# Performance work log

Hardware: AMD Instinct MI355X
Metric: run time of the kernel (lower is better)

Reference implementation:

```python
import jax, jax.numpy as jnp
from jax import lax
import numpy as np

N = 4
ALPHA_AP = 0.85
ALPHA_DS = 0.1
ALPHA_LR = 1.0
C1 = 0.01 ** 2
C2 = 0.03 ** 2


def resize_ac(img, nh, nw):
    # bilinear resize, align_corners=True (matches F.interpolate(..., align_corners=True))
    B, C, H, W = img.shape
    ys = jnp.linspace(0.0, H - 1.0, nh)
    xs = jnp.linspace(0.0, W - 1.0, nw)
    y0 = jnp.floor(ys).astype(jnp.int32)
    y1 = jnp.minimum(y0 + 1, H - 1)
    x0 = jnp.floor(xs).astype(jnp.int32)
    x1 = jnp.minimum(x0 + 1, W - 1)
    wy = (ys - y0).astype(img.dtype)[None, None, :, None]
    wx = (xs - x0).astype(img.dtype)[None, None, None, :]
    top = img[:, :, y0, :] * (1.0 - wy) + img[:, :, y1, :] * wy
    return top[:, :, :, x0] * (1.0 - wx) + top[:, :, :, x1] * wx


def build_pyramid(img):
    B, C, H, W = img.shape
    pyr = [img]
    for i in range(N - 1):
        r = 2 ** (i + 1)
        pyr.append(resize_ac(pyr[i], H // r, W // r))  # resize previous level, as in torch code
    return pyr


def x_grad(img):
    # replicate-pad right then diff -> last column is exactly zero
    g = img[:, :, :, :-1] - img[:, :, :, 1:]
    return jnp.concatenate([g, jnp.zeros_like(img[:, :, :, :1])], axis=3)


def y_grad(img):
    g = img[:, :, :-1, :] - img[:, :, 1:, :]
    return jnp.concatenate([g, jnp.zeros_like(img[:, :, :1, :])], axis=2)


def avgpool3(x):
    # AvgPool2d(3, 1), VALID padding
    return lax.reduce_window(x, 0.0, lax.add, (1, 1, 3, 3), (1, 1, 1, 1), 'VALID') / 9.0


def grid_sample_zeros(img, gx, gy):
    # bilinear grid_sample, padding_mode='zeros', align_corners=True
    B, C, H, W = img.shape
    x = (gx + 1.0) * 0.5 * (W - 1)
    y = (gy + 1.0) * 0.5 * (H - 1)
    x0 = jnp.floor(x)
    y0 = jnp.floor(y)

    def corner(xi, yi, w):
        valid = (xi >= 0) & (xi <= W - 1) & (yi >= 0) & (yi <= H - 1)
        xc = jnp.clip(xi, 0, W - 1).astype(jnp.int32)
        yc = jnp.clip(yi, 0, H - 1).astype(jnp.int32)
        vals = jax.vmap(lambda im, yy, xx: im[:, yy, xx])(img, yc, xc)  # [B,C,H,W]
        return vals * (w * valid.astype(img.dtype))[:, None]

    return (corner(x0, y0, (x0 + 1 - x) * (y0 + 1 - y))
            + corner(x0 + 1, y0, (x - x0) * (y0 + 1 - y))
            + corner(x0, y0 + 1, (x0 + 1 - x) * (y - y0))
            + corner(x0 + 1, y0 + 1, (x - x0) * (y - y0)))


def apply_disparity(img, disp):
    # standard Monodepth bilinear sampler: shift x_base in [0,1] by disp, grid_sample
    B, C, H, W = img.shape
    x_base = jnp.linspace(0.0, 1.0, W)[None, None, :]
    y_base = jnp.linspace(0.0, 1.0, H)[None, :, None]
    gx = 2.0 * (x_base + disp[:, 0]) - 1.0  # [B,H,W]
    gy = jnp.broadcast_to(2.0 * y_base - 1.0, gx.shape)
    return grid_sample_zeros(img, gx, gy)


def dssim(x, y):
    mu_x = avgpool3(x)
    mu_y = avgpool3(y)
    sig_x = avgpool3(x * x) - mu_x ** 2
    sig_y = avgpool3(y * y) - mu_y ** 2
    cov = avgpool3(x * y) - mu_x * mu_y
    ssim = ((2.0 * mu_x * mu_y + C1) * (2.0 * cov + C2)) / ((mu_x ** 2 + mu_y ** 2 + C1) * (sig_x + sig_y + C2))
    return jnp.mean(jnp.clip((1.0 - ssim) / 2.0, 0.0, 1.0))


def smoothness(disp, img, level):
    wx = jnp.exp(-jnp.mean(jnp.abs(x_grad(img)), axis=1, keepdims=True))
    wy = jnp.exp(-jnp.mean(jnp.abs(y_grad(img)), axis=1, keepdims=True))
    sx = x_grad(disp) * wx
    sy = y_grad(disp) * wy
    return jnp.mean(jnp.abs(sx) + jnp.abs(sy)) / (2 ** level)


def loss_forward(disps, left, right):
    lp = build_pyramid(left)
    rp = build_pyramid(right)
    dl = [d[:, 0:1] for d in disps]
    dr = [d[:, 1:2] for d in disps]
    left_est = [apply_disparity(rp[i], -dl[i]) for i in range(N)]
    right_est = [apply_disparity(lp[i], dr[i]) for i in range(N)]
    r2l_disp = [apply_disparity(dr[i], -dl[i]) for i in range(N)]
    l2r_disp = [apply_disparity(dl[i], dr[i]) for i in range(N)]
    # appearance matching (note: outer *ALPHA_AP matches the original's AP_loss*self.alpha_AP)
    AP = sum(ALPHA_AP * dssim(lp[i], left_est[i]) + (1.0 - ALPHA_AP) * jnp.mean(jnp.abs(lp[i] - left_est[i])) for i in range(N))
    AP = AP + sum(ALPHA_AP * dssim(rp[i], right_est[i]) + (1.0 - ALPHA_AP) * jnp.mean(jnp.abs(rp[i] - right_est[i])) for i in range(N))
    AP = AP * ALPHA_AP
    LR = sum(jnp.mean(jnp.abs(dl[i] - r2l_disp[i])) for i in range(N))
    LR = (LR + sum(jnp.mean(jnp.abs(dr[i] - l2r_disp[i])) for i in range(N))) * ALPHA_LR
    DS = sum(smoothness(dl[i], lp[i], i) for i in range(N))
    DS = (DS + sum(smoothness(dr[i], rp[i], i) for i in range(N))) * ALPHA_DS
    total = AP + LR + DS
    return total, AP, LR, DS


def setup_inputs() -> dict:
    key = jax.random.key(0)
    ks = jax.random.split(key, 6)
    B, H, W = 32, 256, 512
    inp = {}
    for i in range(N):
        h, w = H >> i, W >> i
        # normalized disparities in [0, 0.05) as in trained Monodepth
        inp[f'disp{i}'] = jax.random.uniform(ks[i], (B, 2, h, w), jnp.float32) * 0.05
    inp['left'] = jax.random.uniform(ks[4], (B, 3, H, W), jnp.float32)
    inp['right'] = jax.random.uniform(ks[5], (B, 3, H, W), jnp.float32)
    return inp


def reference(disp0, disp1, disp2, disp3, left, right):
    return loss_forward([disp0, disp1, disp2, disp3], left, right)
```

## Files before the change

### kernel.cpp

```cpp
#include <hip/hip_runtime.h>

#define BDIM 256
#define SH 16

struct LevelDesc {
    const float* lp; const float* rp; const float* dp;
    int H, W, nCW, nRS, nPerSide, waveBase;
};
struct AllParams { LevelDesc lv[4]; int totalWaves; };

__global__ void zero_acc_kernel(double* acc) {
    if (threadIdx.x < 32) acc[threadIdx.x] = 0.0;
}

__global__ void resize2_kernel(const float* __restrict__ sL, const float* __restrict__ sR,
                               float* __restrict__ dL, float* __restrict__ dR,
                               int BC, int Hs, int Ws, int Hd, int Wd) {
    long long half = (long long)BC * Hd * Wd;
    long long idx = (long long)blockIdx.x * blockDim.x + threadIdx.x;
    if (idx >= 2 * half) return;
    const float* src = (idx < half) ? sL : sR;
    float* dst = (idx < half) ? dL : dR;
    long long id = (idx < half) ? idx : idx - half;
    int i = (int)(id % Wd);
    long long t = id / Wd;
    int j = (int)(t % Hd);
    int bc = (int)(t / Hd);
    float stepy = (float)(Hs - 1) / (float)(Hd - 1);
    float stepx = (float)(Ws - 1) / (float)(Wd - 1);
    float y = j * stepy;
    float x = i * stepx;
    int y0 = (int)floorf(y);
    int y1 = min(y0 + 1, Hs - 1);
    int x0 = (int)floorf(x);
    int x1 = min(x0 + 1, Ws - 1);
    float wy = y - (float)y0;
    float wx = x - (float)x0;
    const float* s = src + (long long)bc * Hs * Ws;
    float t0 = s[(long long)y0 * Ws + x0] * (1.0f - wy) + s[(long long)y1 * Ws + x0] * wy;
    float t1 = s[(long long)y0 * Ws + x1] * (1.0f - wy) + s[(long long)y1 * Ws + x1] * wy;
    dst[id] = t0 * (1.0f - wx) + t1 * wx;
}

__device__ __forceinline__ float ssim_term(float Sx, float Sy, float Sxx, float Syy, float Sxy) {
    const float C1v = 0.0001f;
    const float C2v = 0.0009f;
    float mux = Sx * (1.0f / 9.0f), muy = Sy * (1.0f / 9.0f);
    float sigx = Sxx * (1.0f / 9.0f) - mux * mux;
    float sigy = Syy * (1.0f / 9.0f) - muy * muy;
    float cov  = Sxy * (1.0f / 9.0f) - mux * muy;
    float num = (2.0f * mux * muy + C1v) * (2.0f * cov + C2v);
    float den = (mux * mux + muy * muy + C1v) * (sigx + sigy + C2v);
    float v = (1.0f - num * __builtin_amdgcn_rcpf(den)) * 0.5f;
    return fminf(fmaxf(v, 0.0f), 1.0f);
}

struct RowVals {
    float d0, d1;
    float xv[3][2];
    float w00, w01, w10, w11;
    float dA, dB, dC, dD;
    float sA[3], sB[3], sC[3], sD[3];
};

__global__ void __launch_bounds__(BDIM)
mega_kernel(AllParams P, double* __restrict__ acc) {
    const int lane = threadIdx.x & 63;
    const int wid  = threadIdx.x >> 6;
    const int wId  = blockIdx.x * (BDIM / 64) + wid;
    const int w = min(wId, P.totalWaves - 1);

    int level = 0;
    if (w >= P.lv[1].waveBase) level = 1;
    if (w >= P.lv[2].waveBase) level = 2;
    if (w >= P.lv[3].waveBase) level = 3;
    LevelDesc L;
    if (level == 0) L = P.lv[0];
    else if (level == 1) L = P.lv[1];
    else if (level == 2) L = P.lv[2];
    else L = P.lv[3];

    int rel = w - L.waveBase;
    const int side = (rel >= L.nPerSide) ? 1 : 0;
    rel -= side * L.nPerSide;
    const int cw = rel % L.nCW; rel /= L.nCW;
    const int rs = rel % L.nRS;
    const int b  = rel / L.nRS;

    const int H = L.H, W = L.W;
    const long long HW = (long long)H * W;
    const unsigned HWu = (unsigned)HW;
    const float Wm1f = (float)(W - 1);
    const float sgn = side ? 1.0f : -1.0f;

    const float* xim = (side ? L.rp : L.lp) + (long long)b * 3 * HW;
    const float* sim = (side ? L.lp : L.rp) + (long long)b * 3 * HW;
    const float* dme = L.dp + (long long)b * 2 * HW + (side ? HW : 0);
    const float* dot = L.dp + (long long)b * 2 * HW + (side ? 0 : HW);

    const int base = cw * 126;
    const int c0 = base + 2 * lane;
    const int c1 = c0 + 1;
    const bool in0 = c0 < W, in1 = c1 < W;
    const int cc = min(c0, W - 2) >> 1;
    const float fc0 = (float)c0, fc1 = (float)c1;

    const bool lastW = (cw == L.nCW - 1);
    const bool own0 = in0 && (c0 < base + 126 || lastW);
    const bool own1 = in1 && (c1 < base + 126 || lastW);
    const bool ownS0 = own0 && (c0 <= W - 3);
    const bool ownS1 = own1 && (c1 <= W - 3);

    const int r0 = rs * SH;
    const int r1 = min(r0 + SH, H);
    const int jend = min(r1 + 1, H - 1);

    float Pst[3][5][2], Lst[3][5][2];
#pragma unroll
    for (int c = 0; c < 3; ++c)
#pragma unroll
        for (int s = 0; s < 5; ++s) { Pst[c][s][0] = 0.f; Pst[c][s][1] = 0.f;
                                      Lst[c][s][0] = 0.f; Lst[c][s][1] = 0.f; }
    float pd0 = 0.f, pd1 = 0.f;
    float pxv[3][2] = {{0.f,0.f},{0.f,0.f},{0.f,0.f}};

    float f_ss = 0.f, f_l1 = 0.f, f_lr = 0.f, f_ds = 0.f;

    auto load_dp = [&](int jj, float& o0, float& o1) {
        float2 dpair = ((const float2*)(dme + (unsigned)jj * (unsigned)W))[cc];
        o0 = dpair.x; o1 = dpair.y;
    };

    auto issue_gathers = [&](float di0, float di1, int jj, RowVals& R) {
        const unsigned ro = (unsigned)jj * (unsigned)W;
        R.d0 = di0; R.d1 = di1;
        float xq0 = fmaf(sgn * di0, Wm1f, fc0);
        float xq1 = fmaf(sgn * di1, Wm1f, fc1);
        float xf0 = floorf(xq0), xf1 = floorf(xq1);
        int g0 = (int)xf0, g1 = (int)xf1;
        float t0 = xq0 - xf0, t1 = xq1 - xf1;
        R.w00 = (g0 >= 0 && g0 < W)         ? 1.0f - t0 : 0.0f;
        R.w01 = (g0 >= -1 && g0 < W - 1)    ? t0        : 0.0f;
        R.w10 = (g1 >= 0 && g1 < W)         ? 1.0f - t1 : 0.0f;
        R.w11 = (g1 >= -1 && g1 < W - 1)    ? t1        : 0.0f;
        unsigned a0 = ro + (unsigned)min(max(g0, 0), W - 1);
        unsigned a1 = ro + (unsigned)min(max(g0 + 1, 0), W - 1);
        unsigned b0 = ro + (unsigned)min(max(g1, 0), W - 1);
        unsigned b1 = ro + (unsigned)min(max(g1 + 1, 0), W - 1);
        R.dA = dot[a0]; R.dB = dot[a1]; R.dC = dot[b0]; R.dD = dot[b1];
#pragma unroll
        for (int c = 0; c < 3; ++c) {
            const unsigned co = (unsigned)c * HWu;
            float2 xp2 = ((const float2*)(xim + co + ro))[cc];
            R.xv[c][0] = in0 ? xp2.x : 0.f;
            R.xv[c][1] = in1 ? xp2.y : 0.f;
            R.sA[c] = sim[co + a0]; R.sB[c] = sim[co + a1];
            R.sC[c] = sim[co + b0]; R.sD[c] = sim[co + b1];
        }
    };

    auto consume = [&](const RowVals& R, int j) {
        const float d0 = R.d0, d1 = R.d1;
        float wv0 = R.dA * R.w00 + R.dB * R.w01;
        float wv1 = R.dC * R.w10 + R.dD * R.w11;
        float xv[3][2], yv[3][2];
#pragma unroll
        for (int c = 0; c < 3; ++c) {
            xv[c][0] = R.xv[c][0]; xv[c][1] = R.xv[c][1];
            float ya = R.sA[c] * R.w00 + R.sB[c] * R.w01;
            float yb = R.sC[c] * R.w10 + R.sD[c] * R.w11;
            yv[c][0] = in0 ? ya : 0.f;
            yv[c][1] = in1 ? yb : 0.f;
        }

        const bool rowOwn = j < r1;
        if (rowOwn) {
            if (own0) {
                f_l1 += fabsf(xv[0][0] - yv[0][0]) + fabsf(xv[1][0] - yv[1][0]) + fabsf(xv[2][0] - yv[2][0]);
                f_lr += fabsf(d0 - wv0);
            }
            if (own1) {
                f_l1 += fabsf(xv[0][1] - yv[0][1]) + fabsf(xv[1][1] - yv[1][1]) + fabsf(xv[2][1] - yv[2][1]);
                f_lr += fabsf(d1 - wv1);
            }
        }

        {
            float dn  = __shfl_down(d0, 1);
            float xn0 = __shfl_down(xv[0][0], 1);
            float xn1 = __shfl_down(xv[1][0], 1);
            float xn2 = __shfl_down(xv[2][0], 1);
            if (rowOwn) {
                if (own0 && c0 < W - 1) {
                    float g = fabsf(xv[0][0] - xv[0][1]) + fabsf(xv[1][0] - xv[1][1]) + fabsf(xv[2][0] - xv[2][1]);
                    f_ds += fabsf((d0 - d1) * __expf(-g * (1.0f / 3.0f)));
                }
                if (own1 && c1 < W - 1) {
                    float g = fabsf(xv[0][1] - xn0) + fabsf(xv[1][1] - xn1) + fabsf(xv[2][1] - xn2);
                    f_ds += fabsf((d1 - dn) * __expf(-g * (1.0f / 3.0f)));
                }
            }
        }
        if (j > r0 && (j - 1) < r1) {
            if (own0) {
                float g = fabsf(pxv[0][0] - xv[0][0]) + fabsf(pxv[1][0] - xv[1][0]) + fabsf(pxv[2][0] - xv[2][0]);
                f_ds += fabsf((pd0 - d0) * __expf(-g * (1.0f / 3.0f)));
            }
            if (own1) {
                float g = fabsf(pxv[0][1] - xv[0][1]) + fabsf(pxv[1][1] - xv[1][1]) + fabsf(pxv[2][1] - xv[2][1]);
                f_ds += fabsf((pd1 - d1) * __expf(-g * (1.0f / 3.0f)));
            }
        }
        pd0 = d0; pd1 = d1;
#pragma unroll
        for (int c = 0; c < 3; ++c) { pxv[c][0] = xv[c][0]; pxv[c][1] = xv[c][1]; }

        const bool emit = (j >= r0 + 2);
#pragma unroll
        for (int c = 0; c < 3; ++c) {
            float cs[5][2];
#pragma unroll
            for (int p = 0; p < 2; ++p) {
                float cx = xv[c][p], cy = yv[c][p];
                float v5[5] = {cx, cy, cx * cx, cy * cy, cx * cy};
#pragma unroll
                for (int s = 0; s < 5; ++s) {
                    cs[s][p] = Pst[c][s][p] + v5[s];
                    Pst[c][s][p] = Lst[c][s][p] + v5[s];
                    Lst[c][s][p] = v5[s];
                }
            }
            if (emit) {
                float w0s[5], w1s[5];
#pragma unroll
                for (int s = 0; s < 5; ++s) {
                    float n0 = __shfl_down(cs[s][0], 1);
                    float n1 = __shfl_down(cs[s][1], 1);
                    w0s[s] = cs[s][0] + cs[s][1] + n0;
                    w1s[s] = cs[s][1] + n0 + n1;
                }
                float ts0 = ssim_term(w0s[0], w0s[1], w0s[2], w0s[3], w0s[4]);
                float ts1 = ssim_term(w1s[0], w1s[1], w1s[2], w1s[3], w1s[4]);
                f_ss += (ownS0 ? ts0 : 0.f) + (ownS1 ? ts1 : 0.f);
            }
        }
    };

    RowVals A, B;
    float dq0, dq1, dn0, dn1;
    load_dp(r0, dq0, dq1);
    load_dp(min(r0 + 1, jend), dn0, dn1);
    issue_gathers(dq0, dq1, r0, A);

    int j = r0;
    for (;;) {
        float dp20, dp21;
        load_dp(min(j + 2, jend), dp20, dp21);
        if (j < jend) issue_gathers(dn0, dn1, j + 1, B);
        consume(A, j);
        dn0 = dp20; dn1 = dp21;
        if (++j > jend) break;

        load_dp(min(j + 2, jend), dp20, dp21);
        if (j < jend) issue_gathers(dn0, dn1, j + 1, A);
        consume(B, j);
        dn0 = dp20; dn1 = dp21;
        if (++j > jend) break;
    }

#pragma unroll
    for (int o = 32; o > 0; o >>= 1) {
        f_ss += __shfl_down(f_ss, o);
        f_l1 += __shfl_down(f_l1, o);
        f_lr += __shfl_down(f_lr, o);
        f_ds += __shfl_down(f_ds, o);
    }
    __shared__ float red[BDIM / 64][4];
    __shared__ int meta[2];
    if (threadIdx.x == 0) { meta[0] = level; meta[1] = side; }
    if (lane == 0) {
        red[wid][0] = f_ss; red[wid][1] = f_l1;
        red[wid][2] = f_lr; red[wid][3] = f_ds;
    }
    __syncthreads();
    if (threadIdx.x < 4) {
        int t = threadIdx.x;
        double s = (double)red[0][t] + (double)red[1][t]
                 + (double)red[2][t] + (double)red[3][t];
        atomicAdd(acc + t * 8 + meta[1] * 4 + meta[0], s);
    }
}

__global__ void finalize_kernel(const double* __restrict__ acc, float* __restrict__ out) {
    const int B = 32, H0 = 256, W0 = 512;
    double AP = 0.0, LR = 0.0, DS = 0.0;
    for (int i = 0; i < 4; ++i) {
        int h = H0 >> i, w = W0 >> i;
        double nss = (double)B * 3.0 * (double)(h - 2) * (double)(w - 2);
        double nl1 = (double)B * 3.0 * (double)h * (double)w;
        double nd  = (double)B * (double)h * (double)w;
        AP += 0.85 * (acc[0 + i] / nss) + 0.15 * (acc[8 + i] / nl1);
        AP += 0.85 * (acc[4 + i] / nss) + 0.15 * (acc[12 + i] / nl1);
        LR += acc[16 + i] / nd + acc[20 + i] / nd;
        double sc = 1.0 / (double)(1 << i);
        DS += (acc[24 + i] / nd) * sc + (acc[28 + i] / nd) * sc;
    }
    AP *= 0.85;
    DS *= 0.1;
    double total = AP + LR + DS;
    out[0] = (float)total;
    out[1] = (float)AP;
    out[2] = (float)LR;
    out[3] = (float)DS;
}

extern "C" void kernel_launch(void* const* d_in, const int* in_sizes, int n_in,
                              void* d_out, int out_size, void* d_ws, size_t ws_size,
                              hipStream_t stream) {
    const int B = 32, H0 = 256, W0 = 512;
    const float* dsp[4];
    for (int i = 0; i < 4; ++i) dsp[i] = (const float*)d_in[i];
    const float* left  = (const float*)d_in[4];
    const float* right = (const float*)d_in[5];
    float* out = (float*)d_out;

    double* acc = (double*)d_ws;
    float* buf = (float*)((char*)d_ws + 256);

    const float* lp[4];
    const float* rp[4];
    float* lpm[4];
    float* rpm[4];
    lp[0] = left; rp[0] = right;
    float* cur = buf;
    for (int i = 1; i < 4; ++i) { lpm[i] = cur; cur += (long long)B * 3 * (H0 >> i) * (W0 >> i); }
    for (int i = 1; i < 4; ++i) { rpm[i] = cur; cur += (long long)B * 3 * (H0 >> i) * (W0 >> i); }
    for (int i = 1; i < 4; ++i) { lp[i] = lpm[i]; rp[i] = rpm[i]; }

    zero_acc_kernel<<<1, 64, 0, stream>>>(acc);

    for (int i = 1; i < 4; ++i) {
        int Hs = H0 >> (i - 1), Ws = W0 >> (i - 1);
        int Hd = H0 >> i, Wd = W0 >> i;
        long long half = (long long)B * 3 * Hd * Wd;
        int g = (int)((2 * half + BDIM - 1) / BDIM);
        resize2_kernel<<<g, BDIM, 0, stream>>>(
            lp[i - 1], rp[i - 1], lpm[i], rpm[i], B * 3, Hs, Ws, Hd, Wd);
    }

    AllParams P;
    int wb = 0;
    for (int i = 0; i < 4; ++i) {
        int h = H0 >> i, w = W0 >> i;
        LevelDesc& L = P.lv[i];
        L.lp = lp[i]; L.rp = rp[i]; L.dp = dsp[i];
        L.H = h; L.W = w;
        L.nCW = (w - 2 + 125) / 126;
        L.nRS = h / SH;
        L.nPerSide = B * L.nRS * L.nCW;
        L.waveBase = wb;
        wb += 2 * L.nPerSide;
    }
    P.totalWaves = wb;
    int blocks = (wb + (BDIM / 64) - 1) / (BDIM / 64);
    mega_kernel<<<blocks, BDIM, 0, stream>>>(P, acc);

    finalize_kernel<<<1, 1, 0, stream>>>(acc, out);
}
```

Baseline: 308.6 us.

## Pack SSIM math into float2 vectors, use DPP shifts, uniform base pointers, fold zeroing

```diff
diff --git a/kernel.cpp b/kernel.cpp
--- a/kernel.cpp
+++ b/kernel.cpp
@@ -2,6 +2,8 @@
 
 #define BDIM 256
 #define SH 16
+
+typedef float v2f __attribute__((ext_vector_type(2)));
 
 struct LevelDesc {
     const float* lp; const float* rp; const float* dp;
@@ -9,13 +11,26 @@
 };
 struct AllParams { LevelDesc lv[4]; int totalWaves; };
 
-__global__ void zero_acc_kernel(double* acc) {
-    if (threadIdx.x < 32) acc[threadIdx.x] = 0.0;
-}
+__device__ __forceinline__ float dpp_shl1(float x) {
+    int r = __builtin_amdgcn_update_dpp(0, __float_as_int(x), 0x130, 0xF, 0xF, true);
+    return __int_as_float(r);
+}
+
+__device__ __forceinline__ const float* uptr(const float* p) {
+    unsigned long long u = (unsigned long long)p;
+    unsigned lo = __builtin_amdgcn_readfirstlane((unsigned)u);
+    unsigned hi = __builtin_amdgcn_readfirstlane((unsigned)(u >> 32));
+    return (const float*)(((unsigned long long)hi << 32) | (unsigned long long)lo);
+}
+
+__device__ __forceinline__ v2f mkv(float a, float b) { v2f r; r.x = a; r.y = b; return r; }
+
 
 __global__ void resize2_kernel(const float* __restrict__ sL, const float* __restrict__ sR,
                                float* __restrict__ dL, float* __restrict__ dR,
-                               int BC, int Hs, int Ws, int Hd, int Wd) {
+                               int BC, int Hs, int Ws, int Hd, int Wd,
+                               double* acc, int doZero) {
+    if (doZero && blockIdx.x == 0 && threadIdx.x < 32) acc[threadIdx.x] = 0.0;
     long long half = (long long)BC * Hd * Wd;
     long long idx = (long long)blockIdx.x * blockDim.x + threadIdx.x;
     if (idx >= 2 * half) return;
@@ -42,25 +57,32 @@
     dst[id] = t0 * (1.0f - wx) + t1 * wx;
 }
 
-__device__ __forceinline__ float ssim_term(float Sx, float Sy, float Sxx, float Syy, float Sxy) {
+__device__ __forceinline__ v2f ssim_term2(v2f Sx, v2f Sy, v2f Sxx, v2f Syy, v2f Sxy) {
     const float C1v = 0.0001f;
     const float C2v = 0.0009f;
-    float mux = Sx * (1.0f / 9.0f), muy = Sy * (1.0f / 9.0f);
-    float sigx = Sxx * (1.0f / 9.0f) - mux * mux;
-    float sigy = Syy * (1.0f / 9.0f) - muy * muy;
-    float cov  = Sxy * (1.0f / 9.0f) - mux * muy;
-    float num = (2.0f * mux * muy + C1v) * (2.0f * cov + C2v);
-    float den = (mux * mux + muy * muy + C1v) * (sigx + sigy + C2v);
-    float v = (1.0f - num * __builtin_amdgcn_rcpf(den)) * 0.5f;
-    return fminf(fmaxf(v, 0.0f), 1.0f);
+    const float i9 = 1.0f / 9.0f;
+    v2f mux = Sx * i9, muy = Sy * i9;
+    v2f sigx = Sxx * i9 - mux * mux;
+    v2f sigy = Syy * i9 - muy * muy;
+    v2f cov  = Sxy * i9 - mux * muy;
+    v2f num = ((2.0f * mux) * muy + C1v) * (2.0f * cov + C2v);
+    v2f den = (mux * mux + muy * muy + C1v) * (sigx + sigy + C2v);
+    v2f r;
+    r.x = __builtin_amdgcn_rcpf(den.x);
+    r.y = __builtin_amdgcn_rcpf(den.y);
+    v2f v = (1.0f - num * r) * 0.5f;
+    v2f o;
+    o.x = fminf(fmaxf(v.x, 0.0f), 1.0f);
+    o.y = fminf(fmaxf(v.y, 0.0f), 1.0f);
+    return o;
 }
 
 struct RowVals {
     float d0, d1;
-    float xv[3][2];
-    float w00, w01, w10, w11;
-    float dA, dB, dC, dD;
-    float sA[3], sB[3], sC[3], sD[3];
+    v2f xv[3];
+    v2f wI, wJ;
+    v2f dI, dJ;
+    v2f sI[3], sJ[3];
 };
 
 __global__ void __launch_bounds__(BDIM)
@@ -93,10 +115,10 @@
     const float Wm1f = (float)(W - 1);
     const float sgn = side ? 1.0f : -1.0f;
 
-    const float* xim = (side ? L.rp : L.lp) + (long long)b * 3 * HW;
-    const float* sim = (side ? L.lp : L.rp) + (long long)b * 3 * HW;
-    const float* dme = L.dp + (long long)b * 2 * HW + (side ? HW : 0);
-    const float* dot = L.dp + (long long)b * 2 * HW + (side ? 0 : HW);
+    const float* xim = uptr((side ? L.rp : L.lp) + (long long)b * 3 * HW);
+    const float* sim = uptr((side ? L.lp : L.rp) + (long long)b * 3 * HW);
+    const float* dme = uptr(L.dp + (long long)b * 2 * HW + (side ? HW : 0));
+    const float* dot = uptr(L.dp + (long long)b * 2 * HW + (side ? 0 : HW));
 
     const int base = cw * 126;
     const int c0 = base + 2 * lane;
@@ -115,14 +137,13 @@
     const int r1 = min(r0 + SH, H);
     const int jend = min(r1 + 1, H - 1);
 
-    float Pst[3][5][2], Lst[3][5][2];
+    v2f Pst[3][5], Lst[3][5];
 #pragma unroll
     for (int c = 0; c < 3; ++c)
 #pragma unroll
-        for (int s = 0; s < 5; ++s) { Pst[c][s][0] = 0.f; Pst[c][s][1] = 0.f;
-                                      Lst[c][s][0] = 0.f; Lst[c][s][1] = 0.f; }
+        for (int s = 0; s < 5; ++s) { Pst[c][s] = mkv(0.f, 0.f); Lst[c][s] = mkv(0.f, 0.f); }
     float pd0 = 0.f, pd1 = 0.f;
-    float pxv[3][2] = {{0.f,0.f},{0.f,0.f},{0.f,0.f}};
+    v2f pxv[3] = {mkv(0.f,0.f), mkv(0.f,0.f), mkv(0.f,0.f)};
 
     float f_ss = 0.f, f_l1 = 0.f, f_lr = 0.f, f_ds = 0.f;
 
@@ -139,109 +160,110 @@
         float xf0 = floorf(xq0), xf1 = floorf(xq1);
         int g0 = (int)xf0, g1 = (int)xf1;
         float t0 = xq0 - xf0, t1 = xq1 - xf1;
-        R.w00 = (g0 >= 0 && g0 < W)         ? 1.0f - t0 : 0.0f;
-        R.w01 = (g0 >= -1 && g0 < W - 1)    ? t0        : 0.0f;
-        R.w10 = (g1 >= 0 && g1 < W)         ? 1.0f - t1 : 0.0f;
-        R.w11 = (g1 >= -1 && g1 < W - 1)    ? t1        : 0.0f;
+        float w00 = (g0 >= 0 && g0 < W)         ? 1.0f - t0 : 0.0f;
+        float w01 = (g0 >= -1 && g0 < W - 1)    ? t0        : 0.0f;
+        float w10 = (g1 >= 0 && g1 < W)         ? 1.0f - t1 : 0.0f;
+        float w11 = (g1 >= -1 && g1 < W - 1)    ? t1        : 0.0f;
+        R.wI = mkv(w00, w10);
+        R.wJ = mkv(w01, w11);
         unsigned a0 = ro + (unsigned)min(max(g0, 0), W - 1);
         unsigned a1 = ro + (unsigned)min(max(g0 + 1, 0), W - 1);
         unsigned b0 = ro + (unsigned)min(max(g1, 0), W - 1);
         unsigned b1 = ro + (unsigned)min(max(g1 + 1, 0), W - 1);
-        R.dA = dot[a0]; R.dB = dot[a1]; R.dC = dot[b0]; R.dD = dot[b1];
+        R.dI = mkv(dot[a0], dot[b0]);
+        R.dJ = mkv(dot[a1], dot[b1]);
 #pragma unroll
         for (int c = 0; c < 3; ++c) {
             const unsigned co = (unsigned)c * HWu;
             float2 xp2 = ((const float2*)(xim + co + ro))[cc];
-            R.xv[c][0] = in0 ? xp2.x : 0.f;
-            R.xv[c][1] = in1 ? xp2.y : 0.f;
-            R.sA[c] = sim[co + a0]; R.sB[c] = sim[co + a1];
-            R.sC[c] = sim[co + b0]; R.sD[c] = sim[co + b1];
+            R.xv[c] = mkv(in0 ? xp2.x : 0.f, in1 ? xp2.y : 0.f);
+            R.sI[c] = mkv(sim[co + a0], sim[co + b0]);
+            R.sJ[c] = mkv(sim[co + a1], sim[co + b1]);
         }
     };
 
     auto consume = [&](const RowVals& R, int j) {
         const float d0 = R.d0, d1 = R.d1;
-        float wv0 = R.dA * R.w00 + R.dB * R.w01;
-        float wv1 = R.dC * R.w10 + R.dD * R.w11;
-        float xv[3][2], yv[3][2];
+        v2f wv2 = R.dI * R.wI + R.dJ * R.wJ;
+        v2f xv[3], yv[3];
 #pragma unroll
         for (int c = 0; c < 3; ++c) {
-            xv[c][0] = R.xv[c][0]; xv[c][1] = R.xv[c][1];
-            float ya = R.sA[c] * R.w00 + R.sB[c] * R.w01;
-            float yb = R.sC[c] * R.w10 + R.sD[c] * R.w11;
-            yv[c][0] = in0 ? ya : 0.f;
-            yv[c][1] = in1 ? yb : 0.f;
+            xv[c] = R.xv[c];
+            v2f y = R.sI[c] * R.wI + R.sJ[c] * R.wJ;
+            yv[c].x = in0 ? y.x : 0.f;
+            yv[c].y = in1 ? y.y : 0.f;
         }
 
         const bool rowOwn = j < r1;
         if (rowOwn) {
             if (own0) {
-                f_l1 += fabsf(xv[0][0] - yv[0][0]) + fabsf(xv[1][0] - yv[1][0]) + fabsf(xv[2][0] - yv[2][0]);
-                f_lr += fabsf(d0 - wv0);
+                f_l1 += fabsf(xv[0].x - yv[0].x) + fabsf(xv[1].x - yv[1].x) + fabsf(xv[2].x - yv[2].x);
+                f_lr += fabsf(d0 - wv2.x);
             }
             if (own1) {
-                f_l1 += fabsf(xv[0][1] - yv[0][1]) + fabsf(xv[1][1] - yv[1][1]) + fabsf(xv[2][1] - yv[2][1]);
-                f_lr += fabsf(d1 - wv1);
+                f_l1 += fabsf(xv[0].y - yv[0].y) + fabsf(xv[1].y - yv[1].y) + fabsf(xv[2].y - yv[2].y);
+                f_lr += fabsf(d1 - wv2.y);
             }
         }
 
         {
-            float dn  = __shfl_down(d0, 1);
-            float xn0 = __shfl_down(xv[0][0], 1);
-            float xn1 = __shfl_down(xv[1][0], 1);
-            float xn2 = __shfl_down(xv[2][0], 1);
+            float dn  = dpp_shl1(d0);
+            float xn0 = dpp_shl1(xv[0].x);
+            float xn1 = dpp_shl1(xv[1].x);
+            float xn2 = dpp_shl1(xv[2].x);
             if (rowOwn) {
                 if (own0 && c0 < W - 1) {
-                    float g = fabsf(xv[0][0] - xv[0][1]) + fabsf(xv[1][0] - xv[1][1]) + fabsf(xv[2][0] - xv[2][1]);
+                    float g = fabsf(xv[0].x - xv[0].y) + fabsf(xv[1].x - xv[1].y) + fabsf(xv[2].x - xv[2].y);
                     f_ds += fabsf((d0 - d1) * __expf(-g * (1.0f / 3.0f)));
                 }
                 if (own1 && c1 < W - 1) {
-                    float g = fabsf(xv[0][1] - xn0) + fabsf(xv[1][1] - xn1) + fabsf(xv[2][1] - xn2);
+                    float g = fabsf(xv[0].y - xn0) + fabsf(xv[1].y - xn1) + fabsf(xv[2].y - xn2);
                     f_ds += fabsf((d1 - dn) * __expf(-g * (1.0f / 3.0f)));
                 }
             }
         }
         if (j > r0 && (j - 1) < r1) {
+            v2f t0 = pxv[0] - xv[0];
+            v2f t1 = pxv[1] - xv[1];
+            v2f t2 = pxv[2] - xv[2];
             if (own0) {
-                float g = fabsf(pxv[0][0] - xv[0][0]) + fabsf(pxv[1][0] - xv[1][0]) + fabsf(pxv[2][0] - xv[2][0]);
+                float g = fabsf(t0.x) + fabsf(t1.x) + fabsf(t2.x);
                 f_ds += fabsf((pd0 - d0) * __expf(-g * (1.0f / 3.0f)));
             }
             if (own1) {
-                float g = fabsf(pxv[0][1] - xv[0][1]) + fabsf(pxv[1][1] - xv[1][1]) + fabsf(pxv[2][1] - xv[2][1]);
+                float g = fabsf(t0.y) + fabsf(t1.y) + fabsf(t2.y);
                 f_ds += fabsf((pd1 - d1) * __expf(-g * (1.0f / 3.0f)));
             }
         }
         pd0 = d0; pd1 = d1;
 #pragma unroll
-        for (int c = 0; c < 3; ++c) { pxv[c][0] = xv[c][0]; pxv[c][1] = xv[c][1]; }
+        for (int c = 0; c < 3; ++c) pxv[c] = xv[c];
 
         const bool emit = (j >= r0 + 2);
 #pragma unroll
         for (int c = 0; c < 3; ++c) {
-            float cs[5][2];
-#pragma unroll
-            for (int p = 0; p < 2; ++p) {
-                float cx = xv[c][p], cy = yv[c][p];
-                float v5[5] = {cx, cy, cx * cx, cy * cy, cx * cy};
+            v2f X = xv[c], Y = yv[c];
+            v2f V[5];
+            V[0] = X; V[1] = Y;
+            V[2] = X * X; V[3] = Y * Y; V[4] = X * Y;
+            v2f cs[5];
+#pragma unroll
+            for (int s = 0; s < 5; ++s) {
+                cs[s] = Pst[c][s] + V[s];
+                Pst[c][s] = Lst[c][s] + V[s];
+                Lst[c][s] = V[s];
+            }
+            if (emit) {
+                v2f Wn[5];
 #pragma unroll
                 for (int s = 0; s < 5; ++s) {
-                    cs[s][p] = Pst[c][s][p] + v5[s];
-                    Pst[c][s][p] = Lst[c][s][p] + v5[s];
-                    Lst[c][s][p] = v5[s];
+                    float n0 = dpp_shl1(cs[s].x);
+                    float n1 = dpp_shl1(cs[s].y);
+                    Wn[s].x = cs[s].x + cs[s].y + n0;
+                    Wn[s].y = cs[s].y + n0 + n1;
                 }
-            }
-            if (emit) {
-                float w0s[5], w1s[5];
-#pragma unroll
-                for (int s = 0; s < 5; ++s) {
-                    float n0 = __shfl_down(cs[s][0], 1);
-                    float n1 = __shfl_down(cs[s][1], 1);
-                    w0s[s] = cs[s][0] + cs[s][1] + n0;
-                    w1s[s] = cs[s][1] + n0 + n1;
-                }
-                float ts0 = ssim_term(w0s[0], w0s[1], w0s[2], w0s[3], w0s[4]);
-                float ts1 = ssim_term(w1s[0], w1s[1], w1s[2], w1s[3], w1s[4]);
-                f_ss += (ownS0 ? ts0 : 0.f) + (ownS1 ? ts1 : 0.f);
+                v2f ts = ssim_term2(Wn[0], Wn[1], Wn[2], Wn[3], Wn[4]);
+                f_ss += (ownS0 ? ts.x : 0.f) + (ownS1 ? ts.y : 0.f);
             }
         }
     };
@@ -337,15 +359,14 @@
     for (int i = 1; i < 4; ++i) { rpm[i] = cur; cur += (long long)B * 3 * (H0 >> i) * (W0 >> i); }
     for (int i = 1; i < 4; ++i) { lp[i] = lpm[i]; rp[i] = rpm[i]; }
 
-    zero_acc_kernel<<<1, 64, 0, stream>>>(acc);
-
     for (int i = 1; i < 4; ++i) {
         int Hs = H0 >> (i - 1), Ws = W0 >> (i - 1);
         int Hd = H0 >> i, Wd = W0 >> i;
         long long half = (long long)B * 3 * Hd * Wd;
         int g = (int)((2 * half + BDIM - 1) / BDIM);
         resize2_kernel<<<g, BDIM, 0, stream>>>(
-            lp[i - 1], rp[i - 1], lpm[i], rpm[i], B * 3, Hs, Ws, Hd, Wd);
+            lp[i - 1], rp[i - 1], lpm[i], rpm[i], B * 3, Hs, Ws, Hd, Wd,
+            acc, (i == 1) ? 1 : 0);
     }
 
     AllParams P;
```

Measured after the change: 287.1 us. 7.0% less time.
